# Kernel tuning notes

Measured on AMD Instinct MI355X. Metric: run time of the kernel, lower is better.

## Reference

```python
import jax, jax.numpy as jnp
import numpy as np

N_GENES = 15135
N_CMT = 1000
HID = 64


def _gcn_norm(edge_index, n):
    # add self-loops, compute symmetric normalization deg^-1/2 * deg^-1/2
    loop = jnp.arange(n, dtype=edge_index.dtype)
    src = jnp.concatenate([edge_index[0], loop])
    dst = jnp.concatenate([edge_index[1], loop])
    deg = jax.ops.segment_sum(jnp.ones_like(src, dtype=jnp.float32), dst, num_segments=n)
    dinv = jnp.where(deg > 0, 1.0 / jnp.sqrt(deg), 0.0)
    return src, dst, dinv[src] * dinv[dst]


def _gcn_conv(x, W, b, src, dst, norm, n):
    h = x @ W                                  # [bs, N, H]
    m = h[:, src, :] * norm[None, :, None]     # gather messages [bs, E, H]
    out = jnp.zeros_like(h).at[:, dst, :].add(m)
    return out + b


def setup_inputs():
    key = jax.random.key(0)
    ks = jax.random.split(key, 16)
    bs, nf, hfc, ncls, E, P = 8, 64, 128, 2, 242160, 120000
    s = 0.05
    return {
        "x": jax.random.normal(ks[0], (bs, N_GENES, nf), jnp.float32),
        "batch": jnp.zeros((bs,), jnp.int32),
        "edge_index": jax.random.randint(ks[1], (2, E), 0, N_GENES),
        "path_row": jax.random.randint(ks[2], (P,), 0, N_GENES),
        "path_col": jax.random.randint(ks[3], (P,), 0, N_CMT),
        "W1": jax.random.normal(ks[4], (nf, HID), jnp.float32) * s,
        "b1": jnp.zeros((HID,), jnp.float32),
        "W2": jax.random.normal(ks[5], (HID, HID), jnp.float32) * s,
        "b2": jnp.zeros((HID,), jnp.float32),
        "W3": jax.random.normal(ks[6], (HID, HID), jnp.float32) * s,
        "b3": jnp.zeros((HID,), jnp.float32),
        "fcW": jax.random.normal(ks[7], (3 * HID, 1), jnp.float32) * s,
        "fcb": jnp.zeros((1,), jnp.float32),
        "l1W": jax.random.normal(ks[8], (N_CMT, hfc), jnp.float32) * s,
        "l1b": jnp.zeros((hfc,), jnp.float32),
        "l2W": jax.random.normal(ks[9], (hfc, ncls), jnp.float32) * s,
        "l2b": jnp.zeros((ncls,), jnp.float32),
    }


def reference(x, batch, edge_index, path_row, path_col,
              W1, b1, W2, b2, W3, b3, fcW, fcb, l1W, l1b, l2W, l2b):
    bs, n = x.shape[0], x.shape[1]
    src, dst, norm = _gcn_norm(edge_index, n)

    x1 = jax.nn.relu(_gcn_conv(x, W1, b1, src, dst, norm, n))
    x2 = jax.nn.relu(_gcn_conv(x1, W2, b2, src, dst, norm, n))
    x3 = jax.nn.relu(_gcn_conv(x2, W3, b3, src, dst, norm, n))
    # mode='cat': torch.stack(xs, -1).view(bs, N, -1) -> layout [..., h*L + l]
    xc = jnp.stack([x1, x2, x3], axis=-1).reshape(bs, n, HID * 3)

    # pathway pooling: scatter_mean(x[row], col) over node axis
    xt = jnp.transpose(xc, (1, 0, 2))            # [N, bs, F]
    g = xt[path_row]                             # [P, bs, F]
    sums = jax.ops.segment_sum(g, path_col, num_segments=N_CMT)
    cnt = jax.ops.segment_sum(jnp.ones_like(path_col, dtype=xc.dtype), path_col, num_segments=N_CMT)
    pooled = sums / jnp.maximum(cnt, 1.0)[:, None, None]   # [n_cmt, bs, F]
    pooled = jnp.transpose(pooled, (1, 0, 2)).reshape(-1, HID * 3)  # [bs*n_cmt, F]

    h = (pooled @ fcW + fcb).reshape(bs, N_CMT)   # fc -> view(-1, n_cmt)
    h = jax.nn.relu(h @ l1W + l1b)                # (dropout is identity in eval)
    h = h @ l2W + l2b
    return jax.nn.log_softmax(h, axis=-1)
```

## Files before the change

kernel.cpp:

```cpp
#include <hip/hip_runtime.h>
#include <hip/hip_bf16.h>
#include <hip/hip_fp16.h>
#include <math.h>

#define HID 64

#if defined(__has_builtin)
#if __has_builtin(__builtin_amdgcn_cvt_pk_f32_fp8) && __has_builtin(__builtin_amdgcn_cvt_pk_fp8_f32)
#define HWFP8 1
#endif
#endif

typedef float vfloat2 __attribute__((ext_vector_type(2)));


__device__ __forceinline__ unsigned short f2bf(float x) {
    unsigned int u = __float_as_uint(x);
    unsigned int r = u + 0x7fffu + ((u >> 16) & 1u);
    return (unsigned short)(r >> 16);
}

#ifndef HWFP8
__device__ __forceinline__ unsigned int enc8_sw(float a) {
    unsigned short hb = __half_as_ushort(__float2half(a));
    unsigned int r = (unsigned int)hb + 0x7fu + ((hb >> 8) & 1u);
    return (r >> 8) & 0xffu;
}
__device__ __forceinline__ float dec8_sw(unsigned int b) {
    return __half2float(__ushort_as_half((unsigned short)(b << 8)));
}
#endif

__device__ __forceinline__ unsigned int enc4(float a, float b, float c, float d) {
#ifdef HWFP8
    int r = __builtin_amdgcn_cvt_pk_fp8_f32(a, b, 0, false);
    r = __builtin_amdgcn_cvt_pk_fp8_f32(c, d, r, true);
    return (unsigned int)r;
#else
    return enc8_sw(a) | (enc8_sw(b) << 8) | (enc8_sw(c) << 16) | (enc8_sw(d) << 24);
#endif
}

__device__ __forceinline__ void dec4(unsigned int w, float* f) {
#ifdef HWFP8
    vfloat2 a = __builtin_amdgcn_cvt_pk_f32_fp8((int)w, false);
    vfloat2 b = __builtin_amdgcn_cvt_pk_f32_fp8((int)w, true);
    f[0] = a.x; f[1] = a.y; f[2] = b.x; f[3] = b.y;
#else
    f[0] = dec8_sw(w & 0xffu); f[1] = dec8_sw((w >> 8) & 0xffu);
    f[2] = dec8_sw((w >> 16) & 0xffu); f[3] = dec8_sw(w >> 24);
#endif
}

__device__ __forceinline__ void dec8(uint2 g, float* f) {
    dec4(g.x, f);
    dec4(g.y, f + 4);
}


__global__ void k_init_deg(int* __restrict__ deg, int N) {
    int i = blockIdx.x * blockDim.x + threadIdx.x;
    if (i < N) deg[i] = 1;
}

__global__ void k_count(const int* __restrict__ idx, int* __restrict__ cnt, int E) {
    int e = blockIdx.x * blockDim.x + threadIdx.x;
    if (e < E) atomicAdd(&cnt[idx[e]], 1);
}

__global__ void k_dinv(const int* __restrict__ deg, float* __restrict__ dinv, int N) {
    int i = blockIdx.x * blockDim.x + threadIdx.x;
    if (i < N) dinv[i] = rsqrtf((float)deg[i]);
}

template<int SUB>
__global__ void k_scan(const int* __restrict__ deg, int* __restrict__ rowoff, int N) {
    __shared__ int part[256];
    int t = threadIdx.x;
    int CH = (N + 255) >> 8;
    int lo = t * CH, hi = min(lo + CH, N);
    if (lo > N) lo = N;
    int sum = 0;
    for (int i = lo; i < hi; ++i) sum += deg[i] - SUB;
    part[t] = sum;
    __syncthreads();
    for (int off = 1; off < 256; off <<= 1) {
        int v = (t >= off) ? part[t - off] : 0;
        __syncthreads();
        part[t] += v;
        __syncthreads();
    }
    int run = (t == 0) ? 0 : part[t - 1];
    for (int i = lo; i < hi; ++i) { rowoff[i] = run; run += deg[i] - SUB; }
    if (t == 255) rowoff[N] = run;
}

__global__ void k_scatter_edges(const int* __restrict__ src, const int* __restrict__ dst,
                                const float* __restrict__ dinv, const int* __restrict__ rowoff,
                                int* __restrict__ fill, int* __restrict__ ssrc,
                                float* __restrict__ snorm, int E) {
    int e = blockIdx.x * blockDim.x + threadIdx.x;
    if (e >= E) return;
    int s = src[e], d = dst[e];
    int pos = rowoff[d] + atomicAdd(&fill[d], 1);
    ssrc[pos]  = s;
    snorm[pos] = dinv[s] * dinv[d];
}

__global__ void k_scatter_cols(const int* __restrict__ prow, const int* __restrict__ pcol,
                               const int* __restrict__ coff, int* __restrict__ cfill,
                               int* __restrict__ crow, int P) {
    int p = blockIdx.x * blockDim.x + threadIdx.x;
    if (p >= P) return;
    int c = pcol[p];
    int pos = coff[c] + atomicAdd(&cfill[c], 1);
    crow[pos] = prow[p];
}


template<int MODE>
__global__ __launch_bounds__(256) void k_gemm_rt(const void* __restrict__ Xv,
                                                 const float* __restrict__ W,
                                                 unsigned int* __restrict__ Yq,
                                                 float S, int N, int rowsTot) {
    __shared__ float sW[64 * 64];
    __shared__ float sXT[64 * 68];
    int t = threadIdx.x;
    int r0 = blockIdx.x * 64;

#pragma unroll
    for (int i = 0; i < 16; ++i) sW[t + i * 256] = W[t + i * 256];

    {
        int row = t & 63;
        int kg = t >> 6;
        int gr = r0 + row;
        bool ok = gr < rowsTot;
        const float* Xf = (const float*)Xv;
        const unsigned short* Xh = (const unsigned short*)Xv;
#pragma unroll
        for (int i = 0; i < 4; ++i) {
            int k = (kg + i * 4) * 4;
            float4 v = make_float4(0.f, 0.f, 0.f, 0.f);
            if (ok) {
                if (MODE == 0) {
                    int n = gr >> 3, b = gr & 7;
                    v = *(const float4*)&Xf[((size_t)b * N + n) * 64 + k];
                } else {
                    ushort4 u = *(const ushort4*)&Xh[(size_t)gr * 64 + k];
                    v.x = __uint_as_float(((unsigned int)u.x) << 16);
                    v.y = __uint_as_float(((unsigned int)u.y) << 16);
                    v.z = __uint_as_float(((unsigned int)u.z) << 16);
                    v.w = __uint_as_float(((unsigned int)u.w) << 16);
                }
            }
            sXT[(k + 0) * 68 + row] = v.x;
            sXT[(k + 1) * 68 + row] = v.y;
            sXT[(k + 2) * 68 + row] = v.z;
            sXT[(k + 3) * 68 + row] = v.w;
        }
    }
    __syncthreads();

    int ci = t & 15, ri = t >> 4;
    float acc[4][4] = {};
#pragma unroll 16
    for (int k = 0; k < 64; ++k) {
        float4 xr = *(const float4*)&sXT[k * 68 + ri * 4];
        float4 wc = *(const float4*)&sW[k * 64 + ci * 4];
        acc[0][0] = fmaf(xr.x, wc.x, acc[0][0]); acc[0][1] = fmaf(xr.x, wc.y, acc[0][1]);
        acc[0][2] = fmaf(xr.x, wc.z, acc[0][2]); acc[0][3] = fmaf(xr.x, wc.w, acc[0][3]);
        acc[1][0] = fmaf(xr.y, wc.x, acc[1][0]); acc[1][1] = fmaf(xr.y, wc.y, acc[1][1]);
        acc[1][2] = fmaf(xr.y, wc.z, acc[1][2]); acc[1][3] = fmaf(xr.y, wc.w, acc[1][3]);
        acc[2][0] = fmaf(xr.z, wc.x, acc[2][0]); acc[2][1] = fmaf(xr.z, wc.y, acc[2][1]);
        acc[2][2] = fmaf(xr.z, wc.z, acc[2][2]); acc[2][3] = fmaf(xr.z, wc.w, acc[2][3]);
        acc[3][0] = fmaf(xr.w, wc.x, acc[3][0]); acc[3][1] = fmaf(xr.w, wc.y, acc[3][1]);
        acc[3][2] = fmaf(xr.w, wc.z, acc[3][2]); acc[3][3] = fmaf(xr.w, wc.w, acc[3][3]);
    }

#pragma unroll
    for (int j = 0; j < 4; ++j) {
        int row = r0 + ri * 4 + j;
        if (row < rowsTot) {
            Yq[(size_t)row * 16 + ci] =
                enc4(acc[j][0] * S, acc[j][1] * S, acc[j][2] * S, acc[j][3] * S);
        }
    }
}

template<int LAYER, bool STORE>
__global__ __launch_bounds__(256) void k_agg(const uint2* __restrict__ Y,
                                             const int* __restrict__ rowoff,
                                             const int* __restrict__ ssrc,
                                             const float* __restrict__ snorm,
                                             const float* __restrict__ dinv,
                                             const float* __restrict__ bias,
                                             const float* __restrict__ fcW,
                                             uint4* __restrict__ O,
                                             float* __restrict__ sArr,
                                             float invS, int N) {
    int n = blockIdx.x * 4 + (threadIdx.x >> 6);
    if (n >= N) return;
    int lane = threadIdx.x & 63;
    int hb = (lane & 7) * 8;
    float bv[8], wv[8];
#pragma unroll
    for (int k = 0; k < 8; ++k) { bv[k] = bias[hb + k]; wv[k] = fcW[3 * (hb + k) + LAYER]; }

    float dn = dinv[n];
    float w0 = dn * dn;
    float acc[8], f[8];
    dec8(Y[(size_t)n * 64 + lane], f);
#pragma unroll
    for (int k = 0; k < 8; ++k) acc[k] = w0 * f[k];

    int beg = rowoff[n], end = rowoff[n + 1];
    int i = beg;
    for (; i + 7 < end; i += 8) {
        int   sI[8];
        float wI[8];
        uint2 g[8];
#pragma unroll
        for (int u = 0; u < 8; ++u) { sI[u] = ssrc[i + u]; wI[u] = snorm[i + u]; }
#pragma unroll
        for (int u = 0; u < 8; ++u) g[u] = Y[(size_t)sI[u] * 64 + lane];
#pragma unroll
        for (int u = 0; u < 8; ++u) {
            dec8(g[u], f);
#pragma unroll
            for (int k = 0; k < 8; ++k) acc[k] = fmaf(wI[u], f[k], acc[k]);
        }
    }
    for (; i < end; ++i) {
        int s = ssrc[i];
        float w = snorm[i];
        dec8(Y[(size_t)s * 64 + lane], f);
#pragma unroll
        for (int k = 0; k < 8; ++k) acc[k] = fmaf(w, f[k], acc[k]);
    }

    float sv = 0.f;
#pragma unroll
    for (int k = 0; k < 8; ++k) {
        float o = fmaxf(fmaf(acc[k], invS, bv[k]), 0.f);
        acc[k] = o;
        sv = fmaf(o, wv[k], sv);
    }
    if (STORE) {
        uint4 o;
        o.x = (unsigned int)f2bf(acc[0]) | ((unsigned int)f2bf(acc[1]) << 16);
        o.y = (unsigned int)f2bf(acc[2]) | ((unsigned int)f2bf(acc[3]) << 16);
        o.z = (unsigned int)f2bf(acc[4]) | ((unsigned int)f2bf(acc[5]) << 16);
        o.w = (unsigned int)f2bf(acc[6]) | ((unsigned int)f2bf(acc[7]) << 16);
        O[(size_t)n * 64 + lane] = o;
    }
    sv += __shfl_down(sv, 4, 64);
    sv += __shfl_down(sv, 2, 64);
    sv += __shfl_down(sv, 1, 64);
    if ((lane & 7) == 0) {
        int b = lane >> 3;
        float* sp = sArr + (size_t)n * 8 + b;
        if (LAYER == 0) *sp = sv;
        else            *sp += sv;
    }
}


__global__ __launch_bounds__(64) void k_poolg(const float* __restrict__ sArr,
                                              const int* __restrict__ coff,
                                              const int* __restrict__ crow,
                                              float* __restrict__ hpoolT) {
    int c = blockIdx.x;
    int lane = threadIdx.x;
    int beg = coff[c], end = coff[c + 1];
    int b = lane & 7;
    float acc = 0.f;
    for (int i = beg + (lane >> 3); i < end; i += 8) {
        int r = crow[i];
        acc += sArr[(size_t)r * 8 + b];
    }
    acc += __shfl_down(acc, 32, 64);
    acc += __shfl_down(acc, 16, 64);
    acc += __shfl_down(acc, 8, 64);
    if (lane < 8) {
        float inv = 1.f / fmaxf((float)(end - beg), 1.f);
        hpoolT[(size_t)c * 8 + b] = acc * inv;
    }
}

__global__ __launch_bounds__(128) void k_l1p(const float* __restrict__ hpoolT,
                                             const float* __restrict__ fcb,
                                             const float* __restrict__ l1W,
                                             float* __restrict__ hpre,
                                             int NC, int HFC, int CHUNK) {
    __shared__ float hl[64];
    int b = blockIdx.y;
    int c0 = blockIdx.x * CHUNK;
    int j = threadIdx.x;
    int cend = min(c0 + CHUNK, NC);
    for (int c = c0 + j; c < cend; c += blockDim.x)
        hl[c - c0] = hpoolT[(size_t)c * 8 + b] + fcb[0];
    __syncthreads();
    float acc = 0.f;
    for (int c = c0; c < cend; ++c) acc = fmaf(hl[c - c0], l1W[(size_t)c * HFC + j], acc);
    atomicAdd(&hpre[(size_t)b * HFC + j], acc);
}

__global__ __launch_bounds__(256) void k_final(const float* __restrict__ hpre,
                                               const float* __restrict__ l1b,
                                               const float* __restrict__ l2W,
                                               const float* __restrict__ l2b,
                                               float* __restrict__ out,
                                               int bs, int HFC, int NCLS) {
    __shared__ float z[64];
    int t = threadIdx.x;
    int g = t >> 4, l16 = t & 15;
    int nout = bs * NCLS;
    float v = 0.f;
    int b = g / NCLS, k = g - b * NCLS;
    if (g < nout) {
        for (int j = l16; j < HFC; j += 16) {
            float h = fmaxf(hpre[(size_t)b * HFC + j] + l1b[j], 0.f);
            v = fmaf(h, l2W[(size_t)j * NCLS + k], v);
        }
    }
    v += __shfl_down(v, 8, 64);
    v += __shfl_down(v, 4, 64);
    v += __shfl_down(v, 2, 64);
    v += __shfl_down(v, 1, 64);
    if (l16 == 0 && g < nout) z[g] = v + l2b[k];
    __syncthreads();
    if (t < bs) {
        float m = -1e30f;
        for (int c = 0; c < NCLS; ++c) m = fmaxf(m, z[t * NCLS + c]);
        float s = 0.f;
        for (int c = 0; c < NCLS; ++c) s += expf(z[t * NCLS + c] - m);
        float lse = m + logf(s);
        for (int c = 0; c < NCLS; ++c) out[t * NCLS + c] = z[t * NCLS + c] - lse;
    }
}


extern "C" void kernel_launch(void* const* d_in, const int* in_sizes, int n_in,
                              void* d_out, int out_size, void* d_ws, size_t ws_size,
                              hipStream_t stream) {
    const float* x   = (const float*)d_in[0];
    const int* eidx  = (const int*)d_in[2];
    const int* prow  = (const int*)d_in[3];
    const int* pcol  = (const int*)d_in[4];
    const float* W1  = (const float*)d_in[5];
    const float* b1  = (const float*)d_in[6];
    const float* W2  = (const float*)d_in[7];
    const float* b2  = (const float*)d_in[8];
    const float* W3  = (const float*)d_in[9];
    const float* b3  = (const float*)d_in[10];
    const float* fcW = (const float*)d_in[11];
    const float* fcb = (const float*)d_in[12];
    const float* l1W = (const float*)d_in[13];
    const float* l1b = (const float*)d_in[14];
    const float* l2W = (const float*)d_in[15];
    const float* l2b = (const float*)d_in[16];
    float* out = (float*)d_out;

    const int bs   = in_sizes[1];
    const int E    = in_sizes[2] / 2;
    const int P    = in_sizes[3];
    const int N    = in_sizes[0] / (bs * HID);
    const int HFC  = in_sizes[14];
    const int NC   = in_sizes[13] / HFC;
    const int NCLS = in_sizes[15] / HFC;
    const int rows = N * bs;

    const int* esrc = eidx;
    const int* edst = eidx + E;

    size_t off = 0;
    auto alloc = [&](size_t bytes) -> void* {
        void* r = (char*)d_ws + off;
        off += (bytes + 255) & ~(size_t)255;
        return r;
    };
    int*   deg    = (int*)  alloc((size_t)N * 4);
    float* dinv   = (float*)alloc((size_t)N * 4);
    int*   rowoff = (int*)  alloc(((size_t)N + 1) * 4);
    int*   fill   = (int*)  alloc((size_t)N * 4);
    int*   ccnt   = (int*)  alloc((size_t)NC * 4);
    int*   coff   = (int*)  alloc(((size_t)NC + 1) * 4);
    int*   cfill  = (int*)  alloc((size_t)NC * 4);
    int*   crow   = (int*)  alloc((size_t)P * 4);
    float* hpoolT = (float*)alloc((size_t)NC * bs * 4);
    float* hpre   = (float*)alloc((size_t)bs * HFC * 4);
    int*   ssrc   = (int*)  alloc((size_t)E * 4);
    float* snorm  = (float*)alloc((size_t)E * 4);
    unsigned int* Yq   = (unsigned int*)alloc((size_t)rows * HID);
    unsigned short* X1 = (unsigned short*)alloc((size_t)rows * HID * 2);
    unsigned short* X2 = (unsigned short*)alloc((size_t)rows * HID * 2);
    float* sArr   = (float*)alloc((size_t)rows * 4);

    hipMemsetAsync(fill, 0, (size_t)N * 4, stream);
    hipMemsetAsync(ccnt, 0, (size_t)NC * 4, stream);
    hipMemsetAsync(cfill, 0, (size_t)NC * 4, stream);
    hipMemsetAsync(hpre, 0, (size_t)bs * HFC * 4, stream);

    int gN = (N + 255) / 256;
    int gE = (E + 255) / 256;
    int gP = (P + 255) / 256;

    k_init_deg<<<gN, 256, 0, stream>>>(deg, N);
    k_count<<<gE, 256, 0, stream>>>(edst, deg, E);
    k_dinv<<<gN, 256, 0, stream>>>(deg, dinv, N);
    k_scan<1><<<1, 256, 0, stream>>>(deg, rowoff, N);
    k_scatter_edges<<<gE, 256, 0, stream>>>(esrc, edst, dinv, rowoff, fill, ssrc, snorm, E);

    k_count<<<gP, 256, 0, stream>>>(pcol, ccnt, P);
    k_scan<0><<<1, 256, 0, stream>>>(ccnt, coff, NC);
    k_scatter_cols<<<gP, 256, 0, stream>>>(prow, pcol, coff, cfill, crow, P);

    const float S1 = 1.f,  iS1 = 1.f;
    const float S2 = 16.f, iS2 = 1.f / 16.f;
    const float S3 = 128.f, iS3 = 1.f / 128.f;

    int gG = (rows + 63) / 64;
    int gA = (N + 3) / 4;
    k_gemm_rt<0><<<gG, 256, 0, stream>>>(x, W1, Yq, S1, N, rows);
    k_agg<0, true><<<gA, 256, 0, stream>>>((const uint2*)Yq, rowoff, ssrc, snorm, dinv, b1, fcW, (uint4*)X1, sArr, iS1, N);
    k_gemm_rt<1><<<gG, 256, 0, stream>>>(X1, W2, Yq, S2, N, rows);
    k_agg<1, true><<<gA, 256, 0, stream>>>((const uint2*)Yq, rowoff, ssrc, snorm, dinv, b2, fcW, (uint4*)X2, sArr, iS2, N);
    k_gemm_rt<1><<<gG, 256, 0, stream>>>(X2, W3, Yq, S3, N, rows);
    k_agg<2, false><<<gA, 256, 0, stream>>>((const uint2*)Yq, rowoff, ssrc, snorm, dinv, b3, fcW, nullptr, sArr, iS3, N);

    k_poolg<<<NC, 64, 0, stream>>>(sArr, coff, crow, hpoolT);

    const int CHUNK = 40;
    dim3 gL1((NC + CHUNK - 1) / CHUNK, bs);
    k_l1p<<<gL1, 128, 0, stream>>>(hpoolT, fcb, l1W, hpre, NC, HFC, CHUNK);
    k_final<<<1, 256, 0, stream>>>(hpre, l1b, l2W, l2b, out, bs, HFC, NCLS);
}
```

Measured before the change: 394.0 us.

## Fuse whole pipeline into one cooperative persistent kernel with grid syncs

Replaces the sequence of roughly fifteen kernel launches and memsets with a single cooperative persistent kernel that runs every stage, separated by grid-wide barriers. Grid-stride loops cover CSR construction, the three GEMM/aggregation layers, pooling and the MLP head. The GEMM now reads weights straight from global memory instead of staging them in shared memory. The aim is to remove launch overhead and inter-kernel gaps, at the cost of grid-sync latency and possibly lower per-stage efficiency.

```diff
diff --git a/kernel.cpp b/kernel.cpp
--- a/kernel.cpp
+++ b/kernel.cpp
@@ -1,7 +1,10 @@
 #include <hip/hip_runtime.h>
+#include <hip/hip_cooperative_groups.h>
 #include <hip/hip_bf16.h>
 #include <hip/hip_fp16.h>
 #include <math.h>
+
+namespace cg = cooperative_groups;
 
 #define HID 64
 
@@ -58,28 +61,339 @@
 }
 
 
+struct MegaArgs {
+    const float* x;
+    const int* esrc; const int* edst;
+    const int* prow; const int* pcol;
+    const float* W1; const float* b1;
+    const float* W2; const float* b2;
+    const float* W3; const float* b3;
+    const float* fcW; const float* fcb;
+    const float* l1W; const float* l1b;
+    const float* l2W; const float* l2b;
+    float* out;
+    int* deg; float* dinv; int* rowoff; int* fill;
+    int* ccnt; int* coff; int* cfill; int* crow;
+    float* hpoolT; float* hpre;
+    int* ssrc; float* snorm;
+    unsigned int* Yq; unsigned short* X1; unsigned short* X2;
+    float* sArr;
+    int N, E, P, NC, HFC, NCLS, rows, bs;
+};
+
+__device__ void scan_block(const int* __restrict__ cnt, int* __restrict__ off, int n, int* part) {
+    int t = threadIdx.x;
+    int CH = (n + 255) >> 8;
+    int lo = min(t * CH, n), hi = min(lo + CH, n);
+    int sum = 0;
+    for (int i = lo; i < hi; ++i) sum += cnt[i];
+    part[t] = sum;
+    __syncthreads();
+    for (int o = 1; o < 256; o <<= 1) {
+        int v = (t >= o) ? part[t - o] : 0;
+        __syncthreads();
+        part[t] += v;
+        __syncthreads();
+    }
+    int run = (t == 0) ? 0 : part[t - 1];
+    for (int i = lo; i < hi; ++i) { off[i] = run; run += cnt[i]; }
+    if (t == 255) off[n] = run;
+}
+
+template<int MODE>
+__device__ void gemm_stage(const void* __restrict__ Xv, const float* __restrict__ W,
+                           unsigned int* __restrict__ Yq, float S,
+                           int N, int rowsTot, float* sXT) {
+    int t = threadIdx.x;
+    int ci = t & 15, ri = t >> 4;
+    int nT = (rowsTot + 63) >> 6;
+    for (int tile = blockIdx.x; tile < nT; tile += gridDim.x) {
+        __syncthreads();
+        int r0 = tile << 6;
+        {
+            int row = t & 63;
+            int kg = t >> 6;
+            int gr = r0 + row;
+            bool ok = gr < rowsTot;
+            const float* Xf = (const float*)Xv;
+            const unsigned short* Xh = (const unsigned short*)Xv;
+#pragma unroll
+            for (int i = 0; i < 4; ++i) {
+                int k = (kg + i * 4) * 4;
+                float4 v = make_float4(0.f, 0.f, 0.f, 0.f);
+                if (ok) {
+                    if (MODE == 0) {
+                        int n = gr >> 3, b = gr & 7;
+                        v = *(const float4*)&Xf[((size_t)b * N + n) * 64 + k];
+                    } else {
+                        ushort4 u = *(const ushort4*)&Xh[(size_t)gr * 64 + k];
+                        v.x = __uint_as_float(((unsigned int)u.x) << 16);
+                        v.y = __uint_as_float(((unsigned int)u.y) << 16);
+                        v.z = __uint_as_float(((unsigned int)u.z) << 16);
+                        v.w = __uint_as_float(((unsigned int)u.w) << 16);
+                    }
+                }
+                sXT[(k + 0) * 68 + row] = v.x;
+                sXT[(k + 1) * 68 + row] = v.y;
+                sXT[(k + 2) * 68 + row] = v.z;
+                sXT[(k + 3) * 68 + row] = v.w;
+            }
+        }
+        __syncthreads();
+        float acc[4][4] = {};
+#pragma unroll 16
+        for (int k = 0; k < 64; ++k) {
+            float4 xr = *(const float4*)&sXT[k * 68 + ri * 4];
+            float4 wc = *(const float4*)&W[k * 64 + ci * 4];
+            acc[0][0] = fmaf(xr.x, wc.x, acc[0][0]); acc[0][1] = fmaf(xr.x, wc.y, acc[0][1]);
+            acc[0][2] = fmaf(xr.x, wc.z, acc[0][2]); acc[0][3] = fmaf(xr.x, wc.w, acc[0][3]);
+            acc[1][0] = fmaf(xr.y, wc.x, acc[1][0]); acc[1][1] = fmaf(xr.y, wc.y, acc[1][1]);
+            acc[1][2] = fmaf(xr.y, wc.z, acc[1][2]); acc[1][3] = fmaf(xr.y, wc.w, acc[1][3]);
+            acc[2][0] = fmaf(xr.z, wc.x, acc[2][0]); acc[2][1] = fmaf(xr.z, wc.y, acc[2][1]);
+            acc[2][2] = fmaf(xr.z, wc.z, acc[2][2]); acc[2][3] = fmaf(xr.z, wc.w, acc[2][3]);
+            acc[3][0] = fmaf(xr.w, wc.x, acc[3][0]); acc[3][1] = fmaf(xr.w, wc.y, acc[3][1]);
+            acc[3][2] = fmaf(xr.w, wc.z, acc[3][2]); acc[3][3] = fmaf(xr.w, wc.w, acc[3][3]);
+        }
+#pragma unroll
+        for (int j = 0; j < 4; ++j) {
+            int row = r0 + ri * 4 + j;
+            if (row < rowsTot)
+                Yq[(size_t)row * 16 + ci] =
+                    enc4(acc[j][0] * S, acc[j][1] * S, acc[j][2] * S, acc[j][3] * S);
+        }
+    }
+}
+
+template<int LAYER, bool STORE>
+__device__ void agg_stage(const uint2* __restrict__ Y, const int* __restrict__ rowoff,
+                          const int* __restrict__ ssrc, const float* __restrict__ snorm,
+                          const float* __restrict__ dinv, const float* __restrict__ bias,
+                          const float* __restrict__ fcW, uint4* __restrict__ O,
+                          float* __restrict__ sArr, float invS, int N) {
+    int wave = threadIdx.x >> 6, lane = threadIdx.x & 63;
+    int hb = (lane & 7) * 8;
+    float bv[8], wv[8];
+#pragma unroll
+    for (int k = 0; k < 8; ++k) { bv[k] = bias[hb + k]; wv[k] = fcW[3 * (hb + k) + LAYER]; }
+    int nQ = (N + 3) >> 2;
+    for (int q = blockIdx.x; q < nQ; q += gridDim.x) {
+        int n = q * 4 + wave;
+        if (n < N) {
+            float dn = dinv[n];
+            float w0 = dn * dn;
+            float acc[8], f[8];
+            dec8(Y[(size_t)n * 64 + lane], f);
+#pragma unroll
+            for (int k = 0; k < 8; ++k) acc[k] = w0 * f[k];
+
+            int beg = rowoff[n], end = rowoff[n + 1];
+            int i = beg;
+            for (; i + 7 < end; i += 8) {
+                int   sI[8];
+                float wI[8];
+                uint2 g[8];
+#pragma unroll
+                for (int u = 0; u < 8; ++u) { sI[u] = ssrc[i + u]; wI[u] = snorm[i + u]; }
+#pragma unroll
+                for (int u = 0; u < 8; ++u) g[u] = Y[(size_t)sI[u] * 64 + lane];
+#pragma unroll
+                for (int u = 0; u < 8; ++u) {
+                    dec8(g[u], f);
+#pragma unroll
+                    for (int k = 0; k < 8; ++k) acc[k] = fmaf(wI[u], f[k], acc[k]);
+                }
+            }
+            for (; i < end; ++i) {
+                int s = ssrc[i];
+                float w = snorm[i];
+                dec8(Y[(size_t)s * 64 + lane], f);
+#pragma unroll
+                for (int k = 0; k < 8; ++k) acc[k] = fmaf(w, f[k], acc[k]);
+            }
+
+            float sv = 0.f;
+#pragma unroll
+            for (int k = 0; k < 8; ++k) {
+                float o = fmaxf(fmaf(acc[k], invS, bv[k]), 0.f);
+                acc[k] = o;
+                sv = fmaf(o, wv[k], sv);
+            }
+            if (STORE) {
+                uint4 o;
+                o.x = (unsigned int)f2bf(acc[0]) | ((unsigned int)f2bf(acc[1]) << 16);
+                o.y = (unsigned int)f2bf(acc[2]) | ((unsigned int)f2bf(acc[3]) << 16);
+                o.z = (unsigned int)f2bf(acc[4]) | ((unsigned int)f2bf(acc[5]) << 16);
+                o.w = (unsigned int)f2bf(acc[6]) | ((unsigned int)f2bf(acc[7]) << 16);
+                O[(size_t)n * 64 + lane] = o;
+            }
+            sv += __shfl_down(sv, 4, 64);
+            sv += __shfl_down(sv, 2, 64);
+            sv += __shfl_down(sv, 1, 64);
+            if ((lane & 7) == 0) {
+                int b = lane >> 3;
+                float* sp = sArr + (size_t)n * 8 + b;
+                if (LAYER == 0) *sp = sv;
+                else            *sp += sv;
+            }
+        }
+    }
+}
+
+__global__ __launch_bounds__(256, 4) void k_mega(MegaArgs a) {
+    cg::grid_group grid = cg::this_grid();
+    __shared__ __align__(16) char smraw[64 * 68 * 4];
+    float* sXT  = (float*)smraw;
+    int*   sSc  = (int*)smraw;
+    float* sHl  = (float*)smraw;
+    float* sZ   = (float*)smraw;
+
+    int t = threadIdx.x;
+    int gth = blockIdx.x * blockDim.x + t;
+    int GT = gridDim.x * blockDim.x;
+
+    for (int i = gth; i < a.N; i += GT) { a.deg[i] = 0; a.fill[i] = 0; }
+    for (int i = gth; i < a.NC; i += GT) { a.ccnt[i] = 0; a.cfill[i] = 0; }
+    for (int i = gth; i < a.bs * a.HFC; i += GT) a.hpre[i] = 0.f;
+    grid.sync();
+
+    for (int e = gth; e < a.E; e += GT) atomicAdd(&a.deg[a.edst[e]], 1);
+    for (int p = gth; p < a.P; p += GT) atomicAdd(&a.ccnt[a.pcol[p]], 1);
+    grid.sync();
+
+    for (int i = gth; i < a.N; i += GT) a.dinv[i] = rsqrtf((float)(a.deg[i] + 1));
+    if (blockIdx.x == 0)      scan_block(a.deg, a.rowoff, a.N, sSc);
+    else if (blockIdx.x == 1) scan_block(a.ccnt, a.coff, a.NC, sSc);
+    grid.sync();
+
+    for (int e = gth; e < a.E; e += GT) {
+        int s = a.esrc[e], d = a.edst[e];
+        int pos = a.rowoff[d] + atomicAdd(&a.fill[d], 1);
+        a.ssrc[pos] = s;
+        a.snorm[pos] = a.dinv[s] * a.dinv[d];
+    }
+    for (int p = gth; p < a.P; p += GT) {
+        int c = a.pcol[p];
+        int pos = a.coff[c] + atomicAdd(&a.cfill[c], 1);
+        a.crow[pos] = a.prow[p];
+    }
+    grid.sync();
+
+    const float S1v = 1.f, S2v = 16.f, S3v = 128.f;
+    gemm_stage<0>(a.x, a.W1, a.Yq, S1v, a.N, a.rows, sXT);
+    grid.sync();
+    agg_stage<0, true>((const uint2*)a.Yq, a.rowoff, a.ssrc, a.snorm, a.dinv, a.b1, a.fcW,
+                       (uint4*)a.X1, a.sArr, 1.f / S1v, a.N);
+    grid.sync();
+    gemm_stage<1>(a.X1, a.W2, a.Yq, S2v, a.N, a.rows, sXT);
+    grid.sync();
+    agg_stage<1, true>((const uint2*)a.Yq, a.rowoff, a.ssrc, a.snorm, a.dinv, a.b2, a.fcW,
+                       (uint4*)a.X2, a.sArr, 1.f / S2v, a.N);
+    grid.sync();
+    gemm_stage<1>(a.X2, a.W3, a.Yq, S3v, a.N, a.rows, sXT);
+    grid.sync();
+    agg_stage<2, false>((const uint2*)a.Yq, a.rowoff, a.ssrc, a.snorm, a.dinv, a.b3, a.fcW,
+                        nullptr, a.sArr, 1.f / S3v, a.N);
+    grid.sync();
+
+    {
+        int lane = t & 63;
+        int b = lane & 7;
+        for (int c = blockIdx.x * 4 + (t >> 6); c < a.NC; c += gridDim.x * 4) {
+            int beg = a.coff[c], end = a.coff[c + 1];
+            float acc = 0.f;
+            for (int i = beg + (lane >> 3); i < end; i += 8) {
+                int r = a.crow[i];
+                acc += a.sArr[(size_t)r * 8 + b];
+            }
+            acc += __shfl_down(acc, 32, 64);
+            acc += __shfl_down(acc, 16, 64);
+            acc += __shfl_down(acc, 8, 64);
+            if (lane < 8) {
+                float inv = 1.f / fmaxf((float)(end - beg), 1.f);
+                a.hpoolT[(size_t)c * 8 + b] = acc * inv;
+            }
+        }
+    }
+    grid.sync();
+
+    {
+        int nCh = (a.NC + 15) >> 4;
+        float fcb0 = a.fcb[0];
+        for (int cc = blockIdx.x; cc < nCh; cc += gridDim.x) {
+            __syncthreads();
+            if (t < 128) {
+                int ci = t >> 3, b = t & 7;
+                int c = cc * 16 + ci;
+                sHl[ci * 8 + b] = (c < a.NC) ? (a.hpoolT[(size_t)c * 8 + b] + fcb0) : 0.f;
+            }
+            __syncthreads();
+            int j = t & 127, bb = t >> 7;
+            float ac0 = 0.f, ac1 = 0.f, ac2 = 0.f, ac3 = 0.f;
+#pragma unroll
+            for (int ci = 0; ci < 16; ++ci) {
+                int c = cc * 16 + ci;
+                float w = (c < a.NC) ? a.l1W[(size_t)c * a.HFC + j] : 0.f;
+                ac0 = fmaf(sHl[ci * 8 + bb + 0], w, ac0);
+                ac1 = fmaf(sHl[ci * 8 + bb + 2], w, ac1);
+                ac2 = fmaf(sHl[ci * 8 + bb + 4], w, ac2);
+                ac3 = fmaf(sHl[ci * 8 + bb + 6], w, ac3);
+            }
+            atomicAdd(&a.hpre[(size_t)(bb + 0) * a.HFC + j], ac0);
+            atomicAdd(&a.hpre[(size_t)(bb + 2) * a.HFC + j], ac1);
+            atomicAdd(&a.hpre[(size_t)(bb + 4) * a.HFC + j], ac2);
+            atomicAdd(&a.hpre[(size_t)(bb + 6) * a.HFC + j], ac3);
+        }
+    }
+    grid.sync();
+
+    if (blockIdx.x == 0) {
+        int g = t >> 4, l16 = t & 15;
+        int nout = a.bs * a.NCLS;
+        float v = 0.f;
+        int b = g / a.NCLS, k = g - b * a.NCLS;
+        if (g < nout) {
+            for (int j = l16; j < a.HFC; j += 16) {
+                float h = fmaxf(a.hpre[(size_t)b * a.HFC + j] + a.l1b[j], 0.f);
+                v = fmaf(h, a.l2W[(size_t)j * a.NCLS + k], v);
+            }
+        }
+        v += __shfl_down(v, 8, 64);
+        v += __shfl_down(v, 4, 64);
+        v += __shfl_down(v, 2, 64);
+        v += __shfl_down(v, 1, 64);
+        __syncthreads();
+        if (l16 == 0 && g < nout) sZ[g] = v + a.l2b[k];
+        __syncthreads();
+        if (t < a.bs) {
+            float m = -1e30f;
+            for (int c = 0; c < a.NCLS; ++c) m = fmaxf(m, sZ[t * a.NCLS + c]);
+            float s = 0.f;
+            for (int c = 0; c < a.NCLS; ++c) s += expf(sZ[t * a.NCLS + c] - m);
+            float lse = m + logf(s);
+            for (int c = 0; c < a.NCLS; ++c) a.out[t * a.NCLS + c] = sZ[t * a.NCLS + c] - lse;
+        }
+    }
+}
+
+
 __global__ void k_init_deg(int* __restrict__ deg, int N) {
     int i = blockIdx.x * blockDim.x + threadIdx.x;
     if (i < N) deg[i] = 1;
 }
-
 __global__ void k_count(const int* __restrict__ idx, int* __restrict__ cnt, int E) {
     int e = blockIdx.x * blockDim.x + threadIdx.x;
     if (e < E) atomicAdd(&cnt[idx[e]], 1);
 }
-
 __global__ void k_dinv(const int* __restrict__ deg, float* __restrict__ dinv, int N) {
     int i = blockIdx.x * blockDim.x + threadIdx.x;
     if (i < N) dinv[i] = rsqrtf((float)deg[i]);
 }
-
 template<int SUB>
 __global__ void k_scan(const int* __restrict__ deg, int* __restrict__ rowoff, int N) {
     __shared__ int part[256];
     int t = threadIdx.x;
     int CH = (N + 255) >> 8;
-    int lo = t * CH, hi = min(lo + CH, N);
-    if (lo > N) lo = N;
+    int lo = min(t * CH, N), hi = min(lo + CH, N);
     int sum = 0;
     for (int i = lo; i < hi; ++i) sum += deg[i] - SUB;
     part[t] = sum;
@@ -94,7 +408,6 @@
     for (int i = lo; i < hi; ++i) { rowoff[i] = run; run += deg[i] - SUB; }
     if (t == 255) rowoff[N] = run;
 }
-
 __global__ void k_scatter_edges(const int* __restrict__ src, const int* __restrict__ dst,
                                 const float* __restrict__ dinv, const int* __restrict__ rowoff,
                                 int* __restrict__ fill, int* __restrict__ ssrc,
@@ -106,7 +419,6 @@
     ssrc[pos]  = s;
     snorm[pos] = dinv[s] * dinv[d];
 }
-
 __global__ void k_scatter_cols(const int* __restrict__ prow, const int* __restrict__ pcol,
                                const int* __restrict__ coff, int* __restrict__ cfill,
                                int* __restrict__ crow, int P) {
@@ -116,21 +428,14 @@
     int pos = coff[c] + atomicAdd(&cfill[c], 1);
     crow[pos] = prow[p];
 }
-
-
 template<int MODE>
 __global__ __launch_bounds__(256) void k_gemm_rt(const void* __restrict__ Xv,
                                                  const float* __restrict__ W,
                                                  unsigned int* __restrict__ Yq,
                                                  float S, int N, int rowsTot) {
-    __shared__ float sW[64 * 64];
     __shared__ float sXT[64 * 68];
     int t = threadIdx.x;
     int r0 = blockIdx.x * 64;
-
-#pragma unroll
-    for (int i = 0; i < 16; ++i) sW[t + i * 256] = W[t + i * 256];
-
     {
         int row = t & 63;
         int kg = t >> 6;
@@ -161,13 +466,12 @@
         }
     }
     __syncthreads();
-
     int ci = t & 15, ri = t >> 4;
     float acc[4][4] = {};
 #pragma unroll 16
     for (int k = 0; k < 64; ++k) {
         float4 xr = *(const float4*)&sXT[k * 68 + ri * 4];
-        float4 wc = *(const float4*)&sW[k * 64 + ci * 4];
+        float4 wc = *(const float4*)&W[k * 64 + ci * 4];
         acc[0][0] = fmaf(xr.x, wc.x, acc[0][0]); acc[0][1] = fmaf(xr.x, wc.y, acc[0][1]);
         acc[0][2] = fmaf(xr.x, wc.z, acc[0][2]); acc[0][3] = fmaf(xr.x, wc.w, acc[0][3]);
         acc[1][0] = fmaf(xr.y, wc.x, acc[1][0]); acc[1][1] = fmaf(xr.y, wc.y, acc[1][1]);
@@ -177,17 +481,13 @@
         acc[3][0] = fmaf(xr.w, wc.x, acc[3][0]); acc[3][1] = fmaf(xr.w, wc.y, acc[3][1]);
         acc[3][2] = fmaf(xr.w, wc.z, acc[3][2]); acc[3][3] = fmaf(xr.w, wc.w, acc[3][3]);
     }
-
 #pragma unroll
     for (int j = 0; j < 4; ++j) {
         int row = r0 + ri * 4 + j;
-        if (row < rowsTot) {
-            Yq[(size_t)row * 16 + ci] =
-                enc4(acc[j][0] * S, acc[j][1] * S, acc[j][2] * S, acc[j][3] * S);
-        }
-    }
-}
-
+        if (row < rowsTot)
+            Yq[(size_t)row * 16 + ci] = enc4(acc[j][0] * S, acc[j][1] * S, acc[j][2] * S, acc[j][3] * S);
+    }
+}
 template<int LAYER, bool STORE>
 __global__ __launch_bounds__(256) void k_agg(const uint2* __restrict__ Y,
                                              const int* __restrict__ rowoff,
@@ -206,14 +506,12 @@
     float bv[8], wv[8];
 #pragma unroll
     for (int k = 0; k < 8; ++k) { bv[k] = bias[hb + k]; wv[k] = fcW[3 * (hb + k) + LAYER]; }
-
     float dn = dinv[n];
     float w0 = dn * dn;
     float acc[8], f[8];
     dec8(Y[(size_t)n * 64 + lane], f);
 #pragma unroll
     for (int k = 0; k < 8; ++k) acc[k] = w0 * f[k];
-
     int beg = rowoff[n], end = rowoff[n + 1];
     int i = beg;
     for (; i + 7 < end; i += 8) {
@@ -238,7 +536,6 @@
 #pragma unroll
         for (int k = 0; k < 8; ++k) acc[k] = fmaf(w, f[k], acc[k]);
     }
-
     float sv = 0.f;
 #pragma unroll
     for (int k = 0; k < 8; ++k) {
@@ -264,8 +561,6 @@
         else            *sp += sv;
     }
 }
-
-
 __global__ __launch_bounds__(64) void k_poolg(const float* __restrict__ sArr,
                                               const int* __restrict__ coff,
                                               const int* __restrict__ crow,
@@ -287,7 +582,6 @@
         hpoolT[(size_t)c * 8 + b] = acc * inv;
     }
 }
-
 __global__ __launch_bounds__(128) void k_l1p(const float* __restrict__ hpoolT,
                                              const float* __restrict__ fcb,
                                              const float* __restrict__ l1W,
@@ -305,7 +599,6 @@
     for (int c = c0; c < cend; ++c) acc = fmaf(hl[c - c0], l1W[(size_t)c * HFC + j], acc);
     atomicAdd(&hpre[(size_t)b * HFC + j], acc);
 }
-
 __global__ __launch_bounds__(256) void k_final(const float* __restrict__ hpre,
                                                const float* __restrict__ l1b,
                                                const float* __restrict__ l2W,
@@ -397,6 +690,30 @@
     unsigned short* X2 = (unsigned short*)alloc((size_t)rows * HID * 2);
     float* sArr   = (float*)alloc((size_t)rows * 4);
 
+    MegaArgs ma;
+    ma.x = x; ma.esrc = esrc; ma.edst = edst; ma.prow = prow; ma.pcol = pcol;
+    ma.W1 = W1; ma.b1 = b1; ma.W2 = W2; ma.b2 = b2; ma.W3 = W3; ma.b3 = b3;
+    ma.fcW = fcW; ma.fcb = fcb; ma.l1W = l1W; ma.l1b = l1b; ma.l2W = l2W; ma.l2b = l2b;
+    ma.out = out;
+    ma.deg = deg; ma.dinv = dinv; ma.rowoff = rowoff; ma.fill = fill;
+    ma.ccnt = ccnt; ma.coff = coff; ma.cfill = cfill; ma.crow = crow;
+    ma.hpoolT = hpoolT; ma.hpre = hpre;
+    ma.ssrc = ssrc; ma.snorm = snorm;
+    ma.Yq = Yq; ma.X1 = X1; ma.X2 = X2; ma.sArr = sArr;
+    ma.N = N; ma.E = E; ma.P = P; ma.NC = NC; ma.HFC = HFC; ma.NCLS = NCLS;
+    ma.rows = rows; ma.bs = bs;
+
+    int maxPerCU = 0;
+    hipError_t qe = hipOccupancyMaxActiveBlocksPerMultiprocessor(&maxPerCU, k_mega, 256, 0);
+    if (qe == hipSuccess && maxPerCU >= 1) {
+        int nBlocks = maxPerCU * 256;
+        if (nBlocks > 2048) nBlocks = 2048;
+        void* params[] = { (void*)&ma };
+        hipError_t le = hipLaunchCooperativeKernel((const void*)k_mega, dim3(nBlocks),
+                                                   dim3(256), params, 0, stream);
+        if (le == hipSuccess) return;
+    }
+
     hipMemsetAsync(fill, 0, (size_t)N * 4, stream);
     hipMemsetAsync(ccnt, 0, (size_t)NC * 4, stream);
     hipMemsetAsync(cfill, 0, (size_t)NC * 4, stream);
```

After: 1.091 ms. 2.77x slower.

## Fuse graph preprocessing kernels and merge workspace memsets into one

Applied to the files above, without the earlier changes.

Collapses the CSR-build preprocessing (degree init, edge/path counting, dinv, two scans, two scatters) into three grid-stride kernels that handle edges and pathway columns together. The four memsets become a single memset over a contiguous zeroed region, with the self-loop moved into the dinv computation. The intent is to cut kernel-launch and serialization overhead in the setup phase. In exchange the scan now runs one block per scan inside a 64-block kernel, so the two scans run concurrently.

```diff
diff --git a/kernel.cpp b/kernel.cpp
--- a/kernel.cpp
+++ b/kernel.cpp
@@ -58,63 +58,65 @@
 }
 
 
-__global__ void k_init_deg(int* __restrict__ deg, int N) {
-    int i = blockIdx.x * blockDim.x + threadIdx.x;
-    if (i < N) deg[i] = 1;
-}
-
-__global__ void k_count(const int* __restrict__ idx, int* __restrict__ cnt, int E) {
-    int e = blockIdx.x * blockDim.x + threadIdx.x;
-    if (e < E) atomicAdd(&cnt[idx[e]], 1);
-}
-
-__global__ void k_dinv(const int* __restrict__ deg, float* __restrict__ dinv, int N) {
-    int i = blockIdx.x * blockDim.x + threadIdx.x;
-    if (i < N) dinv[i] = rsqrtf((float)deg[i]);
-}
-
-template<int SUB>
-__global__ void k_scan(const int* __restrict__ deg, int* __restrict__ rowoff, int N) {
+__global__ __launch_bounds__(256) void k_pre_count(const int* __restrict__ edst, int* __restrict__ deg, int E,
+                                                   const int* __restrict__ pcol, int* __restrict__ ccnt, int P) {
+    int gth = blockIdx.x * blockDim.x + threadIdx.x;
+    int GT = gridDim.x * blockDim.x;
+    for (int e = gth; e < E; e += GT) atomicAdd(&deg[edst[e]], 1);
+    for (int p = gth; p < P; p += GT) atomicAdd(&ccnt[pcol[p]], 1);
+}
+
+__global__ __launch_bounds__(256) void k_pre_scan(const int* __restrict__ deg, int* __restrict__ rowoff, int N,
+                                                  const int* __restrict__ ccnt, int* __restrict__ coff, int NC,
+                                                  float* __restrict__ dinv) {
     __shared__ int part[256];
     int t = threadIdx.x;
-    int CH = (N + 255) >> 8;
-    int lo = t * CH, hi = min(lo + CH, N);
-    if (lo > N) lo = N;
+    int gth = blockIdx.x * blockDim.x + t;
+    int GT = gridDim.x * blockDim.x;
+    for (int i = gth; i < N; i += GT) dinv[i] = rsqrtf((float)(deg[i] + 1));
+
+    const int* cnt = nullptr; int* off = nullptr; int n = 0;
+    if (blockIdx.x == 0)      { cnt = deg;  off = rowoff; n = N; }
+    else if (blockIdx.x == 1) { cnt = ccnt; off = coff;   n = NC; }
+    else return;
+
+    int CH = (n + 255) >> 8;
+    int lo = min(t * CH, n), hi = min(lo + CH, n);
     int sum = 0;
-    for (int i = lo; i < hi; ++i) sum += deg[i] - SUB;
+    for (int i = lo; i < hi; ++i) sum += cnt[i];
     part[t] = sum;
     __syncthreads();
-    for (int off = 1; off < 256; off <<= 1) {
-        int v = (t >= off) ? part[t - off] : 0;
+    for (int o = 1; o < 256; o <<= 1) {
+        int v = (t >= o) ? part[t - o] : 0;
         __syncthreads();
         part[t] += v;
         __syncthreads();
     }
     int run = (t == 0) ? 0 : part[t - 1];
-    for (int i = lo; i < hi; ++i) { rowoff[i] = run; run += deg[i] - SUB; }
-    if (t == 255) rowoff[N] = run;
-}
-
-__global__ void k_scatter_edges(const int* __restrict__ src, const int* __restrict__ dst,
-                                const float* __restrict__ dinv, const int* __restrict__ rowoff,
-                                int* __restrict__ fill, int* __restrict__ ssrc,
-                                float* __restrict__ snorm, int E) {
-    int e = blockIdx.x * blockDim.x + threadIdx.x;
-    if (e >= E) return;
-    int s = src[e], d = dst[e];
-    int pos = rowoff[d] + atomicAdd(&fill[d], 1);
-    ssrc[pos]  = s;
-    snorm[pos] = dinv[s] * dinv[d];
-}
-
-__global__ void k_scatter_cols(const int* __restrict__ prow, const int* __restrict__ pcol,
-                               const int* __restrict__ coff, int* __restrict__ cfill,
-                               int* __restrict__ crow, int P) {
-    int p = blockIdx.x * blockDim.x + threadIdx.x;
-    if (p >= P) return;
-    int c = pcol[p];
-    int pos = coff[c] + atomicAdd(&cfill[c], 1);
-    crow[pos] = prow[p];
+    for (int i = lo; i < hi; ++i) { off[i] = run; run += cnt[i]; }
+    if (t == 255) off[n] = run;
+}
+
+__global__ __launch_bounds__(256) void k_pre_scatter(const int* __restrict__ esrc, const int* __restrict__ edst,
+                                                     const float* __restrict__ dinv, const int* __restrict__ rowoff,
+                                                     int* __restrict__ fill, int* __restrict__ ssrc,
+                                                     float* __restrict__ snorm, int E,
+                                                     const int* __restrict__ prow, const int* __restrict__ pcol,
+                                                     const int* __restrict__ coff, int* __restrict__ cfill,
+                                                     int* __restrict__ crow, int P) {
+    int gth = blockIdx.x * blockDim.x + threadIdx.x;
+    int GT = gridDim.x * blockDim.x;
+    for (int e = gth; e < E; e += GT) {
+        int s = esrc[e], d = edst[e];
+        int pos = rowoff[d] + atomicAdd(&fill[d], 1);
+        ssrc[pos]  = s;
+        snorm[pos] = dinv[s] * dinv[d];
+    }
+    for (int p = gth; p < P; p += GT) {
+        int c = pcol[p];
+        int pos = coff[c] + atomicAdd(&cfill[c], 1);
+        crow[pos] = prow[p];
+    }
 }
 
 
@@ -181,10 +183,9 @@
 #pragma unroll
     for (int j = 0; j < 4; ++j) {
         int row = r0 + ri * 4 + j;
-        if (row < rowsTot) {
+        if (row < rowsTot)
             Yq[(size_t)row * 16 + ci] =
                 enc4(acc[j][0] * S, acc[j][1] * S, acc[j][2] * S, acc[j][3] * S);
-        }
     }
 }
 
@@ -380,16 +381,18 @@
         off += (bytes + 255) & ~(size_t)255;
         return r;
     };
+    char* zbase   = (char*)d_ws;
     int*   deg    = (int*)  alloc((size_t)N * 4);
+    int*   fill   = (int*)  alloc((size_t)N * 4);
+    int*   ccnt   = (int*)  alloc((size_t)NC * 4);
+    int*   cfill  = (int*)  alloc((size_t)NC * 4);
+    float* hpre   = (float*)alloc((size_t)bs * HFC * 4);
+    size_t zspan  = off;
     float* dinv   = (float*)alloc((size_t)N * 4);
     int*   rowoff = (int*)  alloc(((size_t)N + 1) * 4);
-    int*   fill   = (int*)  alloc((size_t)N * 4);
-    int*   ccnt   = (int*)  alloc((size_t)NC * 4);
     int*   coff   = (int*)  alloc(((size_t)NC + 1) * 4);
-    int*   cfill  = (int*)  alloc((size_t)NC * 4);
     int*   crow   = (int*)  alloc((size_t)P * 4);
     float* hpoolT = (float*)alloc((size_t)NC * bs * 4);
-    float* hpre   = (float*)alloc((size_t)bs * HFC * 4);
     int*   ssrc   = (int*)  alloc((size_t)E * 4);
     float* snorm  = (float*)alloc((size_t)E * 4);
     unsigned int* Yq   = (unsigned int*)alloc((size_t)rows * HID);
@@ -397,24 +400,13 @@
     unsigned short* X2 = (unsigned short*)alloc((size_t)rows * HID * 2);
     float* sArr   = (float*)alloc((size_t)rows * 4);
 
-    hipMemsetAsync(fill, 0, (size_t)N * 4, stream);
-    hipMemsetAsync(ccnt, 0, (size_t)NC * 4, stream);
-    hipMemsetAsync(cfill, 0, (size_t)NC * 4, stream);
-    hipMemsetAsync(hpre, 0, (size_t)bs * HFC * 4, stream);
-
-    int gN = (N + 255) / 256;
-    int gE = (E + 255) / 256;
-    int gP = (P + 255) / 256;
-
-    k_init_deg<<<gN, 256, 0, stream>>>(deg, N);
-    k_count<<<gE, 256, 0, stream>>>(edst, deg, E);
-    k_dinv<<<gN, 256, 0, stream>>>(deg, dinv, N);
-    k_scan<1><<<1, 256, 0, stream>>>(deg, rowoff, N);
-    k_scatter_edges<<<gE, 256, 0, stream>>>(esrc, edst, dinv, rowoff, fill, ssrc, snorm, E);
-
-    k_count<<<gP, 256, 0, stream>>>(pcol, ccnt, P);
-    k_scan<0><<<1, 256, 0, stream>>>(ccnt, coff, NC);
-    k_scatter_cols<<<gP, 256, 0, stream>>>(prow, pcol, coff, cfill, crow, P);
+    hipMemsetAsync(zbase, 0, zspan, stream);
+
+    int gPre = 512;
+    k_pre_count<<<gPre, 256, 0, stream>>>(edst, deg, E, pcol, ccnt, P);
+    k_pre_scan<<<64, 256, 0, stream>>>(deg, rowoff, N, ccnt, coff, NC, dinv);
+    k_pre_scatter<<<gPre, 256, 0, stream>>>(esrc, edst, dinv, rowoff, fill, ssrc, snorm, E,
+                                            prow, pcol, coff, cfill, crow, P);
 
     const float S1 = 1.f,  iS1 = 1.f;
     const float S2 = 16.f, iS2 = 1.f / 16.f;
```

After: 377.3 us. -4.3%, faster.
